# Kernel optimization log

Measured on AMD Instinct MI355X. Metric: run time of the kernel, lower is better.

## Reference

```python
import jax, jax.numpy as jnp
import numpy as np

B, L, C = 256, 196, 2048   # batch, conv_att_size, conv_feat_size
E, H, A = 512, 512, 512    # input_encoding_size, lstm_size, att_hidden_size
INITRANGE = 0.1


def _uniform(key, shape):
    return jax.random.uniform(key, shape, jnp.float32, -INITRANGE, INITRANGE)


def setup_inputs() -> dict:
    key = jax.random.key(0)
    ks = jax.random.split(key, 16)
    return {
        "xt": jax.random.normal(ks[0], (B, E), jnp.float32),
        "att_seq": jax.random.normal(ks[1], (B, L, C), jnp.float32),
        "h0": jax.random.normal(ks[2], (1, B, H), jnp.float32),
        "c0": jax.random.normal(ks[3], (1, B, H), jnp.float32),
        # LSTM input projections
        "Wi": _uniform(ks[4], (4 * H, E)), "bi": _uniform(ks[5], (4 * H,)),
        "Wh": _uniform(ks[6], (4 * H, H)), "bh": _uniform(ks[7], (4 * H,)),
        "Wz": _uniform(ks[8], (4 * H, C)), "bz": _uniform(ks[9], (4 * H,)),
        # attention MLP
        "Wa": _uniform(ks[10], (A, C)), "ba": _uniform(ks[11], (A,)),
        "Wha": _uniform(ks[12], (A, H)), "bha": _uniform(ks[13], (A,)),
        "Wo": _uniform(ks[14], (1, A)), "bo": _uniform(ks[15], (1,)),
    }


def reference(xt, att_seq, h0, c0, Wi, bi, Wh, bh, Wz, bz, Wa, ba, Wha, bha, Wo, bo):
    pre_h = h0[-1]  # [B, H]
    pre_c = c0[-1]  # [B, H]

    # attention scoring MLP
    att_linear = jnp.einsum('blc,ac->bla', att_seq, Wa) + ba      # [B, L, A]
    h_linear = pre_h @ Wha.T + bha                                 # [B, A]
    att_h = jnp.tanh(att_linear + h_linear[:, None, :])            # [B, L, A]
    scores = jnp.einsum('bla,a->bl', att_h, Wo[0]) + bo[0]         # [B, L]
    conv_weight = jax.nn.softmax(scores, axis=1)                   # [B, L]

    # weighted sum over attention locations -> context z
    z = jnp.einsum('blc,bl->bc', att_seq, conv_weight)             # [B, C]

    # fused LSTM gates
    all_input_sums = (xt @ Wi.T + bi) + (pre_h @ Wh.T + bh) + (z @ Wz.T + bz)  # [B, 4H]
    gates = jax.nn.sigmoid(all_input_sums[:, :3 * H])
    in_gate = gates[:, :H]
    forget_gate = gates[:, H:2 * H]
    out_gate = gates[:, 2 * H:3 * H]
    in_transform = jnp.tanh(all_input_sums[:, 3 * H:])

    next_c = forget_gate * pre_c + in_gate * in_transform
    next_h = out_gate * jnp.tanh(next_c)
    # dropout is identity in eval mode (deterministic baseline)
    return next_h, next_c
```

## Files before the change

kernel.cpp:

```cpp
#include <hip/hip_runtime.h>
#include <stdint.h>

#define B_ 256
#define L_ 196
#define C_ 2048
#define E_ 512
#define H_ 512
#define A_ 512
#define M_ (B_*L_)

typedef __bf16 bf16x8 __attribute__((ext_vector_type(8)));
typedef float  f32x4  __attribute__((ext_vector_type(4)));

__device__ __forceinline__ unsigned short f2bf(float f) {
    union { float f; unsigned int u; } v; v.f = f;
    unsigned int r = 0x7FFFu + ((v.u >> 16) & 1u);
    return (unsigned short)((v.u + r) >> 16);
}

__device__ __forceinline__ unsigned int pk2(float a, float b) {
    return (unsigned int)f2bf(a) | ((unsigned int)f2bf(b) << 16);
}

__device__ __forceinline__ float tanh_fast(float x) {
    float e = __expf(2.f * x);
    return 1.f - 2.f / (e + 1.f);
}

__device__ __forceinline__ void gload_lds16(const void* g, void* s) {
    __builtin_amdgcn_global_load_lds(
        (const __attribute__((address_space(1))) void*)g,
        (__attribute__((address_space(3))) void*)s, 16, 0, 0);
}


__global__ void k_cvt(const float* __restrict__ src, unsigned short* __restrict__ dst, int n4) {
    int i = blockIdx.x * blockDim.x + threadIdx.x;
    if (i < n4) {
        float4 v = ((const float4*)src)[i];
        ushort4 o; o.x = f2bf(v.x); o.y = f2bf(v.y); o.z = f2bf(v.z); o.w = f2bf(v.w);
        ((ushort4*)dst)[i] = o;
    }
}

__global__ void k_build_wcat(const float* __restrict__ Wi, const float* __restrict__ Wh,
                             const float* __restrict__ Wz, const float* __restrict__ bi,
                             const float* __restrict__ bh, const float* __restrict__ bz,
                             unsigned short* __restrict__ wcat, float* __restrict__ bcat) {
    int j = blockIdx.x;
    int t = threadIdx.x;
    for (int g = t; g < 768; g += 256) {
        int k = g * 4;
        const float* src;
        if (k < 512)       src = Wi + j*512 + k;
        else if (k < 1024) src = Wh + j*512 + (k - 512);
        else               src = Wz + j*2048 + (k - 1024);
        float4 v = *(const float4*)src;
        ushort4 o; o.x = f2bf(v.x); o.y = f2bf(v.y); o.z = f2bf(v.z); o.w = f2bf(v.w);
        *(ushort4*)(wcat + (size_t)j*3072 + k) = o;
    }
    if (t == 0) bcat[j] = bi[j] + bh[j] + bz[j];
}

__global__ void k_build_xcat(const float* __restrict__ xt, const float* __restrict__ preh,
                             unsigned short* __restrict__ xcat) {
    int b = blockIdx.x, t = threadIdx.x;
    const float* src = (t < 128) ? (xt + b*512 + t*4) : (preh + b*512 + (t-128)*4);
    int off = (t < 128) ? (t*4) : (512 + (t-128)*4);
    float4 v = *(const float4*)src;
    ushort4 o; o.x = f2bf(v.x); o.y = f2bf(v.y); o.z = f2bf(v.z); o.w = f2bf(v.w);
    *(ushort4*)(xcat + (size_t)b*3072 + off) = o;
}

__global__ void k_hlin(const float* __restrict__ preh, const float* __restrict__ Wha,
                       const float* __restrict__ bha, const float* __restrict__ ba,
                       float* __restrict__ hlin) {
    __shared__ float ph[512];
    int b = blockIdx.x, t = threadIdx.x;
    ph[t] = preh[b*512 + t];
    __syncthreads();
    float acc = bha[t] + ba[t];
    const float4* wrow = (const float4*)(Wha + (size_t)t*512);
    #pragma unroll 8
    for (int k4 = 0; k4 < 128; ++k4) {
        float4 v = wrow[k4];
        float4 p = *(const float4*)&ph[k4*4];
        acc += v.x*p.x + v.y*p.y + v.z*p.z + v.w*p.w;
    }
    hlin[b*512 + t] = acc;
}


#define VWAIT8 asm volatile("s_waitcnt vmcnt(8)" ::: "memory")
#define VWAIT4 asm volatile("s_waitcnt vmcnt(4)" ::: "memory")
#define VWAIT0 asm volatile("s_waitcnt vmcnt(0)" ::: "memory")
#define LWAIT0 asm volatile("s_waitcnt lgkmcnt(0)" ::: "memory")

#define ISSUE_B(K0, LBN) do { \
    _Pragma("unroll") \
    for (int i_ = 0; i_ < 8; ++i_) \
        gload_lds16(wa + (size_t)(brow0 + i_*64)*C_ + (K0) + bpsC*8, \
                    (LBN) + (size_t)(tid + i_*512)*8); \
} while(0)

#define LOAD_A(K0) do { const float* ga_ = gaBase + (K0); \
    av0 = *(const float4*)(ga_);      av1 = *(const float4*)(ga_ + 4); \
    av2 = *(const float4*)(ga_ + 8);  av3 = *(const float4*)(ga_ + 12); \
} while(0)

#define PACK_A(LAN) do { \
    uint4 w0_ = make_uint4(pk2(av0.x,av0.y), pk2(av0.z,av0.w), pk2(av1.x,av1.y), pk2(av1.z,av1.w)); \
    uint4 w1_ = make_uint4(pk2(av2.x,av2.y), pk2(av2.z,av2.w), pk2(av3.x,av3.y), pk2(av3.z,av3.w)); \
    *(uint4*)&(LAN)[ar*64 + ((app     ^ ars) * 8)] = w0_; \
    *(uint4*)&(LAN)[ar*64 + (((app+1) ^ ars) * 8)] = w1_; \
} while(0)

#define COMPUTE(KK, LA, LB) do { \
    const int c_ = (KK)*4 + lq; \
    bf16x8 af_[4]; \
    _Pragma("unroll") \
    for (int m_ = 0; m_ < 4; ++m_) { \
        int rrow_ = wr*64 + m_*16 + l16; \
        af_[m_] = *(const bf16x8*)&(LA)[rrow_*64 + ((c_ ^ (rrow_ & 7)) * 8)]; } \
    __builtin_amdgcn_s_setprio(1); \
    _Pragma("unroll") \
    for (int n_ = 0; n_ < 8; ++n_) { \
        int brow_ = wc*128 + n_*16 + l16; \
        bf16x8 bf_ = *(const bf16x8*)&(LB)[brow_*64 + ((c_ ^ (brow_ & 7)) * 8)]; \
        _Pragma("unroll") \
        for (int m_ = 0; m_ < 4; ++m_) \
            acc[m_][n_] = __builtin_amdgcn_mfma_f32_16x16x32_bf16(af_[m_], bf_, acc[m_][n_], 0, 0, 0); } \
    __builtin_amdgcn_s_setprio(0); \
} while(0)

__global__ __launch_bounds__(512, 1) void k_scores(
    const float* __restrict__ att,
    const unsigned short* __restrict__ wa,
    const float* __restrict__ hlin,
    const float* __restrict__ wo,
    const float* __restrict__ bo,
    float* __restrict__ scores)
{
    __shared__ unsigned short smem[81920];
    const int tid = threadIdx.x;
    const int w = tid >> 6, l = tid & 63;
    const int l16 = l & 15, lq = l >> 4;
    const int wr = w >> 2, wc = w & 3;
    const int row0 = blockIdx.x * 128;

    const int ar = tid >> 2;
    const int app = (tid & 3) * 2;
    const int ars = ar & 7;
    const float* gaBase = att + (size_t)(row0 + ar)*C_ + app*8;

    const int brow0 = tid >> 3;
    const int bpsC = (tid & 7) ^ ((tid >> 3) & 7);

    f32x4 acc[4][8];
    #pragma unroll
    for (int m = 0; m < 4; ++m)
        #pragma unroll
        for (int n = 0; n < 8; ++n) acc[m][n] = (f32x4){0.f, 0.f, 0.f, 0.f};

    float4 av0, av1, av2, av3;
    unsigned short* lA0 = smem;
    unsigned short* lB0 = smem + 8192;
    unsigned short* lA1 = smem + 40960;
    unsigned short* lB1 = smem + 40960 + 8192;

    LOAD_A(0);
    ISSUE_B(0, lB0);
    VWAIT8;
    PACK_A(lA0);
    LOAD_A(64);
    VWAIT4;
    LWAIT0;
    __builtin_amdgcn_s_barrier();

    for (int kt = 0; kt < 30; ++kt) {
        unsigned short* lA  = (kt & 1) ? lA1 : lA0;
        unsigned short* lB  = (kt & 1) ? lB1 : lB0;
        unsigned short* lAn = (kt & 1) ? lA0 : lA1;
        unsigned short* lBn = (kt & 1) ? lB0 : lB1;
        ISSUE_B((kt + 1) * 64, lBn);
        COMPUTE(0, lA, lB);
        VWAIT8;
        PACK_A(lAn);
        COMPUTE(1, lA, lB);
        LOAD_A((kt + 2) * 64);
        VWAIT4;
        LWAIT0;
        __builtin_amdgcn_s_barrier();
    }

    {
        ISSUE_B(31 * 64, lB1);
        COMPUTE(0, lA0, lB0);
        VWAIT8;
        PACK_A(lA1);
        COMPUTE(1, lA0, lB0);
        VWAIT0;
        LWAIT0;
        __builtin_amdgcn_s_barrier();
    }

    COMPUTE(0, lA1, lB1);
    COMPUTE(1, lA1, lB1);

    __syncthreads();
    float* red = (float*)smem;

    const int colbase = wc*128 + l16;
    float won[8], hlA[8], hlB[8];
    const int bA = row0 / L_;
    const int bB = (row0 + 127) / L_;
    const int rsplit = (bA + 1) * L_;
    #pragma unroll
    for (int n = 0; n < 8; ++n) {
        won[n] = wo[colbase + n*16];
        hlA[n] = hlin[bA*A_ + colbase + n*16];
        hlB[n] = hlin[bB*A_ + colbase + n*16];
    }

    #pragma unroll
    for (int m = 0; m < 4; ++m) {
        #pragma unroll
        for (int r = 0; r < 4; ++r) {
            int lrow = wr*64 + m*16 + lq*4 + r;
            int grow = row0 + lrow;
            bool useB = grow >= rsplit;
            float s = 0.f;
            #pragma unroll
            for (int n = 0; n < 8; ++n) {
                float v = acc[m][n][r] + (useB ? hlB[n] : hlA[n]);
                s += tanh_fast(v) * won[n];
            }
            s += __shfl_xor(s, 1);
            s += __shfl_xor(s, 2);
            s += __shfl_xor(s, 4);
            s += __shfl_xor(s, 8);
            if (l16 == 0) red[wc*128 + lrow] = s;
        }
    }
    __syncthreads();
    if (tid < 128) {
        scores[row0 + tid] = red[tid] + red[128 + tid] + red[256 + tid] + red[384 + tid] + bo[0];
    }
}

__global__ void k_softmax(const float* __restrict__ scores, float* __restrict__ cw) {
    __shared__ float sm[4], ss[4];
    int b = blockIdx.x, t = threadIdx.x, w = t >> 6, l = t & 63;
    float v = (t < L_) ? scores[b*L_ + t] : -1e30f;
    float m = v;
    #pragma unroll
    for (int o = 1; o < 64; o <<= 1) m = fmaxf(m, __shfl_xor(m, o));
    if (l == 0) sm[w] = m;
    __syncthreads();
    m = fmaxf(fmaxf(sm[0], sm[1]), fmaxf(sm[2], sm[3]));
    float e = (t < L_) ? expf(v - m) : 0.f;
    float s = e;
    #pragma unroll
    for (int o = 1; o < 64; o <<= 1) s += __shfl_xor(s, o);
    if (l == 0) ss[w] = s;
    __syncthreads();
    s = ss[0] + ss[1] + ss[2] + ss[3];
    if (t < L_) cw[b*L_ + t] = e / s;
}

__global__ void k_z(const float* __restrict__ att, const float* __restrict__ cw,
                    unsigned short* __restrict__ xcat) {
    __shared__ float w_s[L_];
    int b = blockIdx.y, half = blockIdx.x, t = threadIdx.x;
    if (t < L_) w_s[t] = cw[b*L_ + t];
    __syncthreads();
    int c = half*1024 + t*4;
    const float* base = att + (size_t)b*L_*C_ + c;
    float ax = 0.f, ay = 0.f, az = 0.f, aw = 0.f;
    #pragma unroll 4
    for (int li = 0; li < L_; ++li) {
        float4 v = *(const float4*)(base + (size_t)li*C_);
        float wt = w_s[li];
        ax += wt*v.x; ay += wt*v.y; az += wt*v.z; aw += wt*v.w;
    }
    ushort4 o; o.x = f2bf(ax); o.y = f2bf(ay); o.z = f2bf(az); o.w = f2bf(aw);
    *(ushort4*)(xcat + (size_t)b*3072 + 1024 + c) = o;
}

__global__ __launch_bounds__(256) void k_gemm2(
    const unsigned short* __restrict__ xcat,
    const unsigned short* __restrict__ wcat,
    const float* __restrict__ bcat,
    float* __restrict__ S)
{
    __shared__ unsigned short lA[64 * 64];
    __shared__ unsigned short lB[128 * 64];
    const int tid = threadIdx.x;
    const int w = tid >> 6, l = tid & 63;
    const int l16 = l & 15, lq = l >> 4;
    const int row0 = blockIdx.y * 64;
    const int col0 = blockIdx.x * 128;

    f32x4 acc[4][2];
    #pragma unroll
    for (int m = 0; m < 4; ++m)
        #pragma unroll
        for (int n = 0; n < 2; ++n) acc[m][n] = (f32x4){0.f, 0.f, 0.f, 0.f};

    for (int kt = 0; kt < 48; ++kt) {
        const int k0 = kt * 64;
        __syncthreads();
        #pragma unroll
        for (int i = 0; i < 2; ++i) {
            int g = tid + i*256;
            int r = g >> 3, q = g & 7;
            *(uint4*)&lA[r*64 + ((q ^ (r & 7)) * 8)] =
                *(const uint4*)(xcat + (size_t)(row0 + r)*3072 + k0 + q*8);
        }
        #pragma unroll
        for (int i = 0; i < 4; ++i) {
            int g = tid + i*256;
            int r = g >> 3, q = g & 7;
            *(uint4*)&lB[r*64 + ((q ^ (r & 7)) * 8)] =
                *(const uint4*)(wcat + (size_t)(col0 + r)*3072 + k0 + q*8);
        }
        __syncthreads();

        #pragma unroll
        for (int kk = 0; kk < 2; ++kk) {
            const int c = kk*4 + lq;
            bf16x8 af[4];
            #pragma unroll
            for (int m = 0; m < 4; ++m) {
                int rr = m*16 + l16;
                af[m] = *(const bf16x8*)&lA[rr*64 + ((c ^ (rr & 7)) * 8)];
            }
            #pragma unroll
            for (int n = 0; n < 2; ++n) {
                int br = w*32 + n*16 + l16;
                bf16x8 bfr = *(const bf16x8*)&lB[br*64 + ((c ^ (br & 7)) * 8)];
                #pragma unroll
                for (int m = 0; m < 4; ++m)
                    acc[m][n] = __builtin_amdgcn_mfma_f32_16x16x32_bf16(af[m], bfr, acc[m][n], 0, 0, 0);
            }
        }
    }

    #pragma unroll
    for (int m = 0; m < 4; ++m)
        #pragma unroll
        for (int n = 0; n < 2; ++n)
            #pragma unroll
            for (int r = 0; r < 4; ++r) {
                int grow = row0 + m*16 + lq*4 + r;
                int col = col0 + w*32 + n*16 + l16;
                S[(size_t)grow*2048 + col] = acc[m][n][r] + bcat[col];
            }
}

__global__ void k_lstm(const float* __restrict__ S, const float* __restrict__ prec,
                       float* __restrict__ out) {
    int b = blockIdx.x, h = threadIdx.x;
    float ig = 1.f / (1.f + expf(-S[(size_t)b*2048 + h]));
    float fg = 1.f / (1.f + expf(-S[(size_t)b*2048 + 512 + h]));
    float og = 1.f / (1.f + expf(-S[(size_t)b*2048 + 1024 + h]));
    float gt = tanhf(S[(size_t)b*2048 + 1536 + h]);
    float c = fg * prec[b*512 + h] + ig * gt;
    out[b*512 + h] = og * tanhf(c);
    out[131072 + b*512 + h] = c;
}

extern "C" void kernel_launch(void* const* d_in, const int* in_sizes, int n_in,
                              void* d_out, int out_size, void* d_ws, size_t ws_size,
                              hipStream_t stream) {
    const float* xt  = (const float*)d_in[0];
    const float* att = (const float*)d_in[1];
    const float* h0  = (const float*)d_in[2];
    const float* c0  = (const float*)d_in[3];
    const float* Wi  = (const float*)d_in[4];
    const float* bi  = (const float*)d_in[5];
    const float* Wh  = (const float*)d_in[6];
    const float* bh  = (const float*)d_in[7];
    const float* Wz  = (const float*)d_in[8];
    const float* bz  = (const float*)d_in[9];
    const float* Wa  = (const float*)d_in[10];
    const float* ba  = (const float*)d_in[11];
    const float* Wha = (const float*)d_in[12];
    const float* bha = (const float*)d_in[13];
    const float* Wo  = (const float*)d_in[14];
    const float* bo  = (const float*)d_in[15];
    float* out = (float*)d_out;

    char* ws = (char*)d_ws;
    unsigned short* wa_bf   = (unsigned short*)(ws);
    unsigned short* wcat_bf = (unsigned short*)(ws + 2097152);
    unsigned short* xcat_bf = (unsigned short*)(ws + 14680064);
    float* hlin   = (float*)(ws + 16252928);
    float* scores = (float*)(ws + 16777216);
    float* cw     = (float*)(ws + 16977920);
    float* bcat   = (float*)(ws + 17178624);
    float* S      = (float*)(ws + 17186816);

    k_cvt<<<1024, 256, 0, stream>>>(Wa, wa_bf, 262144);
    k_build_wcat<<<2048, 256, 0, stream>>>(Wi, Wh, Wz, bi, bh, bz, wcat_bf, bcat);
    k_build_xcat<<<256, 256, 0, stream>>>(xt, h0, xcat_bf);
    k_hlin<<<256, 512, 0, stream>>>(h0, Wha, bha, ba, hlin);
    k_scores<<<M_/128, 512, 0, stream>>>(att, wa_bf, hlin, Wo, bo, scores);
    k_softmax<<<256, 256, 0, stream>>>(scores, cw);
    k_z<<<dim3(2, 256), 256, 0, stream>>>(att, cw, xcat_bf);
    k_gemm2<<<dim3(16, 4), 256, 0, stream>>>(xcat_bf, wcat_bf, bcat, S);
    k_lstm<<<256, 512, 0, stream>>>(S, c0, out);
}
```

Measured before the change: 332.1 us.

## Halve K-tile to 32 and shrink LDS footprint in attention-score GEMM

After: 1.100 ms. +231.1%, slower.

```diff
diff --git a/kernel.cpp b/kernel.cpp
--- a/kernel.cpp
+++ b/kernel.cpp
@@ -91,49 +91,49 @@
 }
 
 
-#define VWAIT8 asm volatile("s_waitcnt vmcnt(8)" ::: "memory")
 #define VWAIT4 asm volatile("s_waitcnt vmcnt(4)" ::: "memory")
+#define VWAIT2 asm volatile("s_waitcnt vmcnt(2)" ::: "memory")
 #define VWAIT0 asm volatile("s_waitcnt vmcnt(0)" ::: "memory")
 #define LWAIT0 asm volatile("s_waitcnt lgkmcnt(0)" ::: "memory")
 
 #define ISSUE_B(K0, LBN) do { \
     _Pragma("unroll") \
-    for (int i_ = 0; i_ < 8; ++i_) \
-        gload_lds16(wa + (size_t)(brow0 + i_*64)*C_ + (K0) + bpsC*8, \
+    for (int i_ = 0; i_ < 4; ++i_) \
+        gload_lds16(wa + (size_t)(brow0 + i_*128)*C_ + (K0) + bq*8, \
                     (LBN) + (size_t)(tid + i_*512)*8); \
 } while(0)
 
 #define LOAD_A(K0) do { const float* ga_ = gaBase + (K0); \
-    av0 = *(const float4*)(ga_);      av1 = *(const float4*)(ga_ + 4); \
-    av2 = *(const float4*)(ga_ + 8);  av3 = *(const float4*)(ga_ + 12); \
+    av0 = *(const float4*)(ga_);  av1 = *(const float4*)(ga_ + 4); \
 } while(0)
 
 #define PACK_A(LAN) do { \
     uint4 w0_ = make_uint4(pk2(av0.x,av0.y), pk2(av0.z,av0.w), pk2(av1.x,av1.y), pk2(av1.z,av1.w)); \
-    uint4 w1_ = make_uint4(pk2(av2.x,av2.y), pk2(av2.z,av2.w), pk2(av3.x,av3.y), pk2(av3.z,av3.w)); \
-    *(uint4*)&(LAN)[ar*64 + ((app     ^ ars) * 8)] = w0_; \
-    *(uint4*)&(LAN)[ar*64 + (((app+1) ^ ars) * 8)] = w1_; \
+    *(uint4*)&(LAN)[aoff] = w0_; \
 } while(0)
 
-#define COMPUTE(KK, LA, LB) do { \
-    const int c_ = (KK)*4 + lq; \
+#define COMPUTE(LA, LB) do { \
     bf16x8 af_[4]; \
     _Pragma("unroll") \
     for (int m_ = 0; m_ < 4; ++m_) { \
-        int rrow_ = wr*64 + m_*16 + l16; \
-        af_[m_] = *(const bf16x8*)&(LA)[rrow_*64 + ((c_ ^ (rrow_ & 7)) * 8)]; } \
+        int rr_ = wr*64 + m_*16 + l16; \
+        int sr_ = rr_ >> 1; \
+        int p_ = lq + 4*(rr_ & 1); \
+        af_[m_] = *(const bf16x8*)&(LA)[sr_*64 + ((p_ ^ (sr_ & 7)) * 8)]; } \
     __builtin_amdgcn_s_setprio(1); \
     _Pragma("unroll") \
     for (int n_ = 0; n_ < 8; ++n_) { \
-        int brow_ = wc*128 + n_*16 + l16; \
-        bf16x8 bf_ = *(const bf16x8*)&(LB)[brow_*64 + ((c_ ^ (brow_ & 7)) * 8)]; \
+        int br_ = wc*128 + n_*16 + l16; \
+        int bsr_ = br_ >> 1; \
+        int bp_ = lq + 4*(br_ & 1); \
+        bf16x8 bf_ = *(const bf16x8*)&(LB)[bsr_*64 + ((bp_ ^ (bsr_ & 7)) * 8)]; \
         _Pragma("unroll") \
         for (int m_ = 0; m_ < 4; ++m_) \
             acc[m_][n_] = __builtin_amdgcn_mfma_f32_16x16x32_bf16(af_[m_], bf_, acc[m_][n_], 0, 0, 0); } \
     __builtin_amdgcn_s_setprio(0); \
 } while(0)
 
-__global__ __launch_bounds__(512, 1) void k_scores(
+__global__ __launch_bounds__(512, 4) void k_scores(
     const float* __restrict__ att,
     const unsigned short* __restrict__ wa,
     const float* __restrict__ hlin,
@@ -141,7 +141,7 @@
     const float* __restrict__ bo,
     float* __restrict__ scores)
 {
-    __shared__ unsigned short smem[81920];
+    __shared__ unsigned short smem[40960];
     const int tid = threadIdx.x;
     const int w = tid >> 6, l = tid & 63;
     const int l16 = l & 15, lq = l >> 4;
@@ -149,12 +149,14 @@
     const int row0 = blockIdx.x * 128;
 
     const int ar = tid >> 2;
-    const int app = (tid & 3) * 2;
-    const int ars = ar & 7;
-    const float* gaBase = att + (size_t)(row0 + ar)*C_ + app*8;
-
-    const int brow0 = tid >> 3;
-    const int bpsC = (tid & 7) ^ ((tid >> 3) & 7);
+    const int aq = tid & 3;
+    const int asr = ar >> 1;
+    const int aoff = asr*64 + (((aq + 4*(ar & 1)) ^ (asr & 7)) * 8);
+    const float* gaBase = att + (size_t)(row0 + ar)*C_ + aq*8;
+
+    const int bp = (tid & 7) ^ ((tid >> 3) & 7);
+    const int brow0 = ((tid >> 3) << 1) + (bp >> 2);
+    const int bq = bp & 3;
 
     f32x4 acc[4][8];
     #pragma unroll
@@ -162,50 +164,47 @@
         #pragma unroll
         for (int n = 0; n < 8; ++n) acc[m][n] = (f32x4){0.f, 0.f, 0.f, 0.f};
 
-    float4 av0, av1, av2, av3;
+    float4 av0, av1;
     unsigned short* lA0 = smem;
-    unsigned short* lB0 = smem + 8192;
-    unsigned short* lA1 = smem + 40960;
-    unsigned short* lB1 = smem + 40960 + 8192;
+    unsigned short* lB0 = smem + 4096;
+    unsigned short* lA1 = smem + 20480;
+    unsigned short* lB1 = smem + 20480 + 4096;
 
     LOAD_A(0);
     ISSUE_B(0, lB0);
-    VWAIT8;
+    VWAIT4;
     PACK_A(lA0);
-    LOAD_A(64);
-    VWAIT4;
+    LOAD_A(32);
+    VWAIT2;
     LWAIT0;
     __builtin_amdgcn_s_barrier();
 
-    for (int kt = 0; kt < 30; ++kt) {
+    for (int kt = 0; kt < 62; ++kt) {
         unsigned short* lA  = (kt & 1) ? lA1 : lA0;
         unsigned short* lB  = (kt & 1) ? lB1 : lB0;
         unsigned short* lAn = (kt & 1) ? lA0 : lA1;
         unsigned short* lBn = (kt & 1) ? lB0 : lB1;
-        ISSUE_B((kt + 1) * 64, lBn);
-        COMPUTE(0, lA, lB);
-        VWAIT8;
+        ISSUE_B((kt + 1) * 32, lBn);
+        COMPUTE(lA, lB);
+        VWAIT4;
         PACK_A(lAn);
-        COMPUTE(1, lA, lB);
-        LOAD_A((kt + 2) * 64);
-        VWAIT4;
+        LOAD_A((kt + 2) * 32);
+        VWAIT2;
         LWAIT0;
         __builtin_amdgcn_s_barrier();
     }
 
     {
-        ISSUE_B(31 * 64, lB1);
-        COMPUTE(0, lA0, lB0);
-        VWAIT8;
+        ISSUE_B(63 * 32, lB1);
+        COMPUTE(lA0, lB0);
+        VWAIT4;
         PACK_A(lA1);
-        COMPUTE(1, lA0, lB0);
         VWAIT0;
         LWAIT0;
         __builtin_amdgcn_s_barrier();
     }
 
-    COMPUTE(0, lA1, lB1);
-    COMPUTE(1, lA1, lB1);
+    COMPUTE(lA1, lB1);
 
     __syncthreads();
     float* red = (float*)smem;
```
